# Optimization experiments

Measured on AMD Instinct MI355X. Metric: run time of the kernel, lower is better.

The kernel has to match this reference:

```python
import jax, jax.numpy as jnp
import numpy as np

B, L, D = 4, 2048, 64
N_HEAD = 4
LOCALITY = 0.2
PI = 3.141592653589793


def setup_inputs() -> dict:
    key = jax.random.key(0)
    k1, k2, k3 = jax.random.split(key, 3)
    mesh = jax.random.uniform(k1, (B, L, 2), dtype=jnp.float32)
    inputs = jax.random.normal(k2, (B, L, D), dtype=jnp.float32)
    lmda = jax.random.uniform(k3, (N_HEAD, 1, 1), dtype=jnp.float32)
    return {"mesh": mesh, "inputs": inputs, "lmda": lmda}


def reference(mesh, inputs, lmda):
    FMAX = jnp.finfo(jnp.float32).max
    # pairwise squared distances: (B, L, L)
    diff = mesh[:, :, None, :] - mesh[:, None, :, :]
    m_dist = jnp.sum(diff * diff, axis=-1)
    # per-head scale in (0, inf): tan(pi/4 * (1-eps) * (1 + sin(lmda)))
    scale = jnp.tan(0.25 * PI * (1.0 - 1e-07) * (1.0 + jnp.sin(lmda)))  # (H,1,1)
    scaled = m_dist[:, None, :, :] * scale  # (B, H, L, L)
    # row-wise quantile threshold (linear interpolation, matching torch.quantile)
    thresh = jnp.quantile(scaled, LOCALITY, axis=-1, keepdims=True)  # (B,H,L,1)
    masked = jnp.where(scaled <= thresh, scaled, FMAX)
    att = jax.nn.softmax(-masked, axis=-1)  # (B, H, L, L)
    # aggregate: (B,H,L,L) x (B,L,D) -> (B,L,H,D) -> (B,L,H*D)
    conv = jnp.einsum('bhnj,bjd->bnhd', att, inputs)
    conv = conv.reshape(inputs.shape[0], -1, N_HEAD * inputs.shape[-1])
    return jnp.concatenate([inputs, conv], axis=-1)
```

## Files before the change

### kernel.cpp

```cpp
#include <hip/hip_runtime.h>
#include <math.h>

#ifndef M_PI
#define M_PI 3.14159265358979323846
#endif

namespace {
constexpr int B_ = 4;
constexpr int L_ = 2048;
constexpr int D_ = 64;
constexpr int H_ = 4;
constexpr int RB = 16;
constexpr int KT = 64;
constexpr int NTILE = L_ / KT;
constexpr int CAPC = 256;
constexpr int OUTW = D_ + H_ * D_;
constexpr int APS = 2064;
}

typedef __attribute__((ext_vector_type(8))) short bf16x8;
typedef __attribute__((ext_vector_type(4))) float f32x4;

__device__ __forceinline__ unsigned bf16_rne(float x) {
    unsigned u = __float_as_uint(x);
    return (u + 0x7fffu + ((u >> 16) & 1u)) >> 16;
}

#define LDS_FENCE() __builtin_amdgcn_s_waitcnt(0xC07F)

__global__ __launch_bounds__(512, 8) void posatt_kernel(
    const float* __restrict__ mesh,
    const float* __restrict__ inputs,
    const float* __restrict__ lmda,
    float* __restrict__ out)
{
    __shared__ __align__(16) float2 s_mesh[L_];
    __shared__ __align__(16) char s_u1[16448];
    __shared__ float s_scale[H_];
    __shared__ float s_th[RB][H_];
    __shared__ float s_d409[RB], s_d410[RB];
    __shared__ float s_wsum[RB][H_];
    __shared__ unsigned s_ccw[8];

    const int t = threadIdx.x;
    const int l = t & 63;
    const int w = t >> 6;
    const int blk = blockIdx.x;
    const int b = blk >> 7;
    const int n0 = (blk & 127) * RB;

    if (t < H_) {
        const double lam = (double)lmda[t];
        const float C = (float)(0.25 * M_PI * (1.0 - 1e-07));
        const float s1 = (float)sin(lam);
        const float arg = __fmul_rn(C, __fadd_rn(1.0f, s1));
        s_scale[t] = (float)tan((double)arg);
    }
    {
        const float4* mg = reinterpret_cast<const float4*>(mesh + (size_t)b * L_ * 2);
        float4* msd = reinterpret_cast<float4*>(s_mesh);
        msd[t] = mg[t];
        msd[t + 512] = mg[t + 512];
    }
    __syncthreads();

    {
        unsigned* hw = reinterpret_cast<unsigned*>(s_u1) + w * 256;
        float* cw = reinterpret_cast<float*>(s_u1 + 8192) + w * CAPC;
        for (int rr = 0; rr < 2; ++rr) {
            const int rl = w * 2 + rr;
            const float2 me = s_mesh[n0 + rl];
            *reinterpret_cast<uint4*>(&hw[l * 4]) = make_uint4(0u, 0u, 0u, 0u);
            if (l == 0) s_ccw[w] = 0u;
            LDS_FENCE();
            #pragma unroll 1
            for (int it = 0; it < 32; ++it) {
                const int j = (it << 6) + l;
                const float2 mj = s_mesh[j];
                const float dx = __fsub_rn(me.x, mj.x);
                const float dy = __fsub_rn(me.y, mj.y);
                const float d = __fadd_rn(__fmul_rn(dx, dx), __fmul_rn(dy, dy));
                int bin = (int)(d * 128.0f); bin = bin < 255 ? bin : 255;
                atomicAdd(&hw[bin], 1u);
            }
            LDS_FENCE();
            const uint4 hv = *reinterpret_cast<const uint4*>(&hw[l * 4]);
            const unsigned p0 = hv.x, p1 = p0 + hv.y, p2 = p1 + hv.z, p3 = p2 + hv.w;
            unsigned sc = p3;
            #pragma unroll
            for (int off = 1; off < 64; off <<= 1) {
                const unsigned uu = __shfl_up(sc, off);
                if (l >= off) sc += uu;
            }
            const unsigned eb = sc - p3;
            const unsigned cum[4] = {eb + p0, eb + p1, eb + p2, eb + p3};
            int flo = -1, fhi = -1; unsigned fbase = 0u;
            #pragma unroll
            for (int e = 0; e < 4; ++e) {
                const unsigned prev = e ? cum[e - 1] : eb;
                if (cum[e] > 409u && prev <= 409u) { flo = l * 4 + e; fbase = prev; }
                if (cum[e] > 410u && prev <= 410u) { fhi = l * 4 + e; }
            }
            const unsigned long long bmlo = __ballot(flo >= 0);
            const int srclo = (int)__builtin_ctzll(bmlo);
            const int lo = __shfl(flo, srclo);
            const unsigned base = __shfl(fbase, srclo);
            const unsigned long long bmhi = __ballot(fhi >= 0);
            const int hi = __shfl(fhi, (int)__builtin_ctzll(bmhi));
            #pragma unroll 1
            for (int it = 0; it < 32; ++it) {
                const int j = (it << 6) + l;
                const float2 mj = s_mesh[j];
                const float dx = __fsub_rn(me.x, mj.x);
                const float dy = __fsub_rn(me.y, mj.y);
                const float d = __fadd_rn(__fmul_rn(dx, dx), __fmul_rn(dy, dy));
                int bin = (int)(d * 128.0f); bin = bin < 255 ? bin : 255;
                if (bin >= lo && bin <= hi) {
                    const unsigned p = atomicAdd(&s_ccw[w], 1u);
                    if (p < (unsigned)CAPC) cw[p] = d;
                }
            }
            LDS_FENCE();
            const int m = (int)min(s_ccw[w], (unsigned)CAPC);
            const int k409 = 409 - (int)base;
            const int k410 = 410 - (int)base;
            #pragma unroll 1
            for (int cc0 = 0; cc0 < m; cc0 += 64) {
                const int ci = cc0 + l;
                const float v = (ci < m) ? cw[ci] : 0.0f;
                int lt = 0, le = 0;
                #pragma unroll 1
                for (int i = 0; i < m; ++i) {
                    const float u = cw[i];
                    lt += (u < v) ? 1 : 0;
                    le += (u <= v) ? 1 : 0;
                }
                if (ci < m) {
                    if (lt <= k409 && k409 < le) s_d409[rl] = v;
                    if (lt <= k410 && k410 < le) s_d410[rl] = v;
                }
            }
            LDS_FENCE();
        }
    }
    __syncthreads();

    if (t < RB * H_) {
        const int r = t >> 2, h = t & 3;
        const float scl = s_scale[h];
        const float s409 = __fmul_rn(s_d409[r], scl);
        const float s410 = __fmul_rn(s_d410[r], scl);
        const float pos = 0.2f * 2047.0f;
        const float g = pos - 409.0f;
        const float lw = 1.0f - g;
        s_th[r][h] = __fadd_rn(__fmul_rn(s409, lw), __fmul_rn(s410, g));
    }
    __syncthreads();

    const int rl_b = t >> 5;
    const int h_b  = (t >> 3) & 3;
    const int jg   = t & 7;
    const float2 me_b = s_mesh[n0 + rl_b];
    const float sc_b = s_scale[h_b];
    const float th_b = s_th[rl_b][h_b];
    float wacc = 0.0f;

    const int hw_ = w >> 1;
    const int kq  = w & 1;
    f32x4 acc[4];
    #pragma unroll
    for (int nq = 0; nq < 4; ++nq) acc[nq] = (f32x4)0.0f;

    const float* inpb = inputs + (size_t)b * L_ * D_;
    char* Abase = s_u1;
    char* Bbase = s_u1 + 4 * APS;

    #pragma unroll 1
    for (int tile = 0; tile < NTILE; ++tile) {
        __syncthreads();
        unsigned pk0[4];
        {
            const int kb0 = tile * KT + ((t >> 6) << 3);
            const float* pb0 = inpb + (size_t)kb0 * D_ + (t & 63);
            #pragma unroll
            for (int e2 = 0; e2 < 4; ++e2) {
                const float xa = pb0[(2 * e2) * D_];
                const float xb = pb0[(2 * e2 + 1) * D_];
                pk0[e2] = bf16_rne(xa) | (bf16_rne(xb) << 16);
            }
        }
        const int k0 = tile * KT;
        #pragma unroll
        for (int m = 0; m < 4; ++m) {
            const int jl = (m << 4) + (jg << 1);
            const float4 mq = *reinterpret_cast<const float4*>(&s_mesh[k0 + jl]);
            const float dx0 = __fsub_rn(me_b.x, mq.x);
            const float dy0 = __fsub_rn(me_b.y, mq.y);
            const float d0 = __fadd_rn(__fmul_rn(dx0, dx0), __fmul_rn(dy0, dy0));
            const float dx1 = __fsub_rn(me_b.x, mq.z);
            const float dy1 = __fsub_rn(me_b.y, mq.w);
            const float d1 = __fadd_rn(__fmul_rn(dx1, dx1), __fmul_rn(dy1, dy1));
            const float x0 = __fmul_rn(d0, sc_b);
            const float x1 = __fmul_rn(d1, sc_b);
            const float e0 = __expf(-x0);
            const float e1 = __expf(-x1);
            const float w0 = (x0 <= th_b) ? e0 : 0.0f;
            const float w1 = (x1 <= th_b) ? e1 : 0.0f;
            wacc += w0 + w1;
            const unsigned u0 = bf16_rne(w0);
            const unsigned u1 = bf16_rne(w1);
            const int ktl = m >> 1;
            const int ql = ((m << 1) + (jg >> 2)) & 3;
            const int chunk = (ktl * 4 + ql) * 16 + rl_b;
            *reinterpret_cast<unsigned*>(Abase + h_b * APS + chunk * 16 + ((jg & 3) << 2)) = u0 | (u1 << 16);
        }
        *reinterpret_cast<uint4*>(Bbase + t * 16) = make_uint4(pk0[0], pk0[1], pk0[2], pk0[3]);
        __syncthreads();
        bf16x8 bfr[4];
        #pragma unroll
        for (int nq = 0; nq < 4; ++nq) {
            bfr[nq] = *reinterpret_cast<const bf16x8*>(
                Bbase + ((kq * 4 + (l >> 4)) * 64 + nq * 16 + (l & 15)) * 16);
        }
        const bf16x8 afr = *reinterpret_cast<const bf16x8*>(
            Abase + hw_ * APS + ((kq * 4 + (l >> 4)) * 16 + (l & 15)) * 16);
        #pragma unroll
        for (int nq = 0; nq < 4; ++nq) {
            acc[nq] = __builtin_amdgcn_mfma_f32_16x16x32_bf16(afr, bfr[nq], acc[nq], 0, 0, 0);
        }
    }
    __syncthreads();

    wacc += __shfl_xor(wacc, 1);
    wacc += __shfl_xor(wacc, 2);
    wacc += __shfl_xor(wacc, 4);
    if ((l & 7) == 0) s_wsum[rl_b][h_b] = wacc;
    {
        float4* Cz = reinterpret_cast<float4*>(s_u1);
        Cz[t] = make_float4(0.f, 0.f, 0.f, 0.f);
        Cz[t + 512] = make_float4(0.f, 0.f, 0.f, 0.f);
    }
    __syncthreads();
    {
        float* Cf = reinterpret_cast<float*>(s_u1);
        #pragma unroll
        for (int nq = 0; nq < 4; ++nq) {
            #pragma unroll
            for (int reg = 0; reg < 4; ++reg) {
                const int row = (l >> 4) * 4 + reg;
                const int col = l & 15;
                atomicAdd(&Cf[((hw_ * 4 + nq) * 16 + row) * 16 + col], acc[nq][reg]);
            }
        }
    }
    __syncthreads();
    {
        const float* Cf = reinterpret_cast<const float*>(s_u1);
        const int r = t >> 5;
        const int c0 = (t & 31) << 3;
        const int h = c0 >> 6;
        const int nq = (c0 >> 4) & 3;
        const int cl = c0 & 15;
        const float wsv = s_wsum[r][h];
        const float inv = (wsv != 0.0f) ? 1.0f / wsv : 0.0f;
        const float* src = &Cf[((h * 4 + nq) * 16 + r) * 16 + cl];
        float4 r0 = *reinterpret_cast<const float4*>(src);
        float4 r1 = *reinterpret_cast<const float4*>(src + 4);
        r0.x *= inv; r0.y *= inv; r0.z *= inv; r0.w *= inv;
        r1.x *= inv; r1.y *= inv; r1.z *= inv; r1.w *= inv;
        float* op = out + (size_t)(b * L_ + n0 + r) * OUTW + D_ + c0;
        *reinterpret_cast<float4*>(op) = r0;
        *reinterpret_cast<float4*>(op + 4) = r1;
    }
    {
        const int r = t >> 5;
        const int c0 = (t & 31) << 1;
        const float2 v = *reinterpret_cast<const float2*>(
            inputs + ((size_t)b * L_ + n0 + r) * D_ + c0);
        *reinterpret_cast<float2*>(out + (size_t)(b * L_ + n0 + r) * OUTW + c0) = v;
    }
}

extern "C" void kernel_launch(void* const* d_in, const int* in_sizes, int n_in,
                              void* d_out, int out_size, void* d_ws, size_t ws_size,
                              hipStream_t stream) {
    const float* mesh   = (const float*)d_in[0];
    const float* inputs = (const float*)d_in[1];
    const float* lmda   = (const float*)d_in[2];
    float* out = (float*)d_out;
    (void)in_sizes; (void)n_in; (void)out_size; (void)d_ws; (void)ws_size;
    hipLaunchKernelGGL(posatt_kernel, dim3(B_ * (L_ / RB)), dim3(512), 0, stream,
                       mesh, inputs, lmda, out);
}
```

Baseline: 145.1 us.

## Halve rows per block and pack two heads into each 16-row MFMA tile

Rows per block drop from 16 to 8, which doubles the grid to 1024 blocks. Each wave now computes the quantile threshold for a single row instead of two. The MFMA A operand is rebuilt so two heads' 8 rows fill one 16-row tile, and waves split along head-pair, K-half and N-half. The aim is to shorten each block's serial threshold phase and spread the work over more CUs, at the cost of reloading mesh and the input tiles twice as often across blocks.

```diff
diff --git a/kernel.cpp b/kernel.cpp
--- a/kernel.cpp
+++ b/kernel.cpp
@@ -10,7 +10,7 @@
 constexpr int L_ = 2048;
 constexpr int D_ = 64;
 constexpr int H_ = 4;
-constexpr int RB = 16;
+constexpr int RB = 8;
 constexpr int KT = 64;
 constexpr int NTILE = L_ / KT;
 constexpr int CAPC = 256;
@@ -46,8 +46,8 @@
     const int l = t & 63;
     const int w = t >> 6;
     const int blk = blockIdx.x;
-    const int b = blk >> 7;
-    const int n0 = (blk & 127) * RB;
+    const int b = blk >> 8;
+    const int n0 = (blk & 255) * RB;
 
     if (t < H_) {
         const double lam = (double)lmda[t];
@@ -67,80 +67,77 @@
     {
         unsigned* hw = reinterpret_cast<unsigned*>(s_u1) + w * 256;
         float* cw = reinterpret_cast<float*>(s_u1 + 8192) + w * CAPC;
-        for (int rr = 0; rr < 2; ++rr) {
-            const int rl = w * 2 + rr;
-            const float2 me = s_mesh[n0 + rl];
-            *reinterpret_cast<uint4*>(&hw[l * 4]) = make_uint4(0u, 0u, 0u, 0u);
-            if (l == 0) s_ccw[w] = 0u;
-            LDS_FENCE();
+        const int rl = w;
+        const float2 me = s_mesh[n0 + rl];
+        *reinterpret_cast<uint4*>(&hw[l * 4]) = make_uint4(0u, 0u, 0u, 0u);
+        if (l == 0) s_ccw[w] = 0u;
+        LDS_FENCE();
+        #pragma unroll 1
+        for (int it = 0; it < 32; ++it) {
+            const int j = (it << 6) + l;
+            const float2 mj = s_mesh[j];
+            const float dx = __fsub_rn(me.x, mj.x);
+            const float dy = __fsub_rn(me.y, mj.y);
+            const float d = __fadd_rn(__fmul_rn(dx, dx), __fmul_rn(dy, dy));
+            int bin = (int)(d * 128.0f); bin = bin < 255 ? bin : 255;
+            atomicAdd(&hw[bin], 1u);
+        }
+        LDS_FENCE();
+        const uint4 hv = *reinterpret_cast<const uint4*>(&hw[l * 4]);
+        const unsigned p0 = hv.x, p1 = p0 + hv.y, p2 = p1 + hv.z, p3 = p2 + hv.w;
+        unsigned sc = p3;
+        #pragma unroll
+        for (int off = 1; off < 64; off <<= 1) {
+            const unsigned uu = __shfl_up(sc, off);
+            if (l >= off) sc += uu;
+        }
+        const unsigned eb = sc - p3;
+        const unsigned cum[4] = {eb + p0, eb + p1, eb + p2, eb + p3};
+        int flo = -1, fhi = -1; unsigned fbase = 0u;
+        #pragma unroll
+        for (int e = 0; e < 4; ++e) {
+            const unsigned prev = e ? cum[e - 1] : eb;
+            if (cum[e] > 409u && prev <= 409u) { flo = l * 4 + e; fbase = prev; }
+            if (cum[e] > 410u && prev <= 410u) { fhi = l * 4 + e; }
+        }
+        const unsigned long long bmlo = __ballot(flo >= 0);
+        const int srclo = (int)__builtin_ctzll(bmlo);
+        const int lo = __shfl(flo, srclo);
+        const unsigned base = __shfl(fbase, srclo);
+        const unsigned long long bmhi = __ballot(fhi >= 0);
+        const int hi = __shfl(fhi, (int)__builtin_ctzll(bmhi));
+        #pragma unroll 1
+        for (int it = 0; it < 32; ++it) {
+            const int j = (it << 6) + l;
+            const float2 mj = s_mesh[j];
+            const float dx = __fsub_rn(me.x, mj.x);
+            const float dy = __fsub_rn(me.y, mj.y);
+            const float d = __fadd_rn(__fmul_rn(dx, dx), __fmul_rn(dy, dy));
+            int bin = (int)(d * 128.0f); bin = bin < 255 ? bin : 255;
+            if (bin >= lo && bin <= hi) {
+                const unsigned p = atomicAdd(&s_ccw[w], 1u);
+                if (p < (unsigned)CAPC) cw[p] = d;
+            }
+        }
+        LDS_FENCE();
+        const int m = (int)min(s_ccw[w], (unsigned)CAPC);
+        const int k409 = 409 - (int)base;
+        const int k410 = 410 - (int)base;
+        #pragma unroll 1
+        for (int cc0 = 0; cc0 < m; cc0 += 64) {
+            const int ci = cc0 + l;
+            const float v = (ci < m) ? cw[ci] : 0.0f;
+            int lt = 0, le = 0;
             #pragma unroll 1
-            for (int it = 0; it < 32; ++it) {
-                const int j = (it << 6) + l;
-                const float2 mj = s_mesh[j];
-                const float dx = __fsub_rn(me.x, mj.x);
-                const float dy = __fsub_rn(me.y, mj.y);
-                const float d = __fadd_rn(__fmul_rn(dx, dx), __fmul_rn(dy, dy));
-                int bin = (int)(d * 128.0f); bin = bin < 255 ? bin : 255;
-                atomicAdd(&hw[bin], 1u);
-            }
-            LDS_FENCE();
-            const uint4 hv = *reinterpret_cast<const uint4*>(&hw[l * 4]);
-            const unsigned p0 = hv.x, p1 = p0 + hv.y, p2 = p1 + hv.z, p3 = p2 + hv.w;
-            unsigned sc = p3;
-            #pragma unroll
-            for (int off = 1; off < 64; off <<= 1) {
-                const unsigned uu = __shfl_up(sc, off);
-                if (l >= off) sc += uu;
-            }
-            const unsigned eb = sc - p3;
-            const unsigned cum[4] = {eb + p0, eb + p1, eb + p2, eb + p3};
-            int flo = -1, fhi = -1; unsigned fbase = 0u;
-            #pragma unroll
-            for (int e = 0; e < 4; ++e) {
-                const unsigned prev = e ? cum[e - 1] : eb;
-                if (cum[e] > 409u && prev <= 409u) { flo = l * 4 + e; fbase = prev; }
-                if (cum[e] > 410u && prev <= 410u) { fhi = l * 4 + e; }
-            }
-            const unsigned long long bmlo = __ballot(flo >= 0);
-            const int srclo = (int)__builtin_ctzll(bmlo);
-            const int lo = __shfl(flo, srclo);
-            const unsigned base = __shfl(fbase, srclo);
-            const unsigned long long bmhi = __ballot(fhi >= 0);
-            const int hi = __shfl(fhi, (int)__builtin_ctzll(bmhi));
-            #pragma unroll 1
-            for (int it = 0; it < 32; ++it) {
-                const int j = (it << 6) + l;
-                const float2 mj = s_mesh[j];
-                const float dx = __fsub_rn(me.x, mj.x);
-                const float dy = __fsub_rn(me.y, mj.y);
-                const float d = __fadd_rn(__fmul_rn(dx, dx), __fmul_rn(dy, dy));
-                int bin = (int)(d * 128.0f); bin = bin < 255 ? bin : 255;
-                if (bin >= lo && bin <= hi) {
-                    const unsigned p = atomicAdd(&s_ccw[w], 1u);
-                    if (p < (unsigned)CAPC) cw[p] = d;
-                }
-            }
-            LDS_FENCE();
-            const int m = (int)min(s_ccw[w], (unsigned)CAPC);
-            const int k409 = 409 - (int)base;
-            const int k410 = 410 - (int)base;
-            #pragma unroll 1
-            for (int cc0 = 0; cc0 < m; cc0 += 64) {
-                const int ci = cc0 + l;
-                const float v = (ci < m) ? cw[ci] : 0.0f;
-                int lt = 0, le = 0;
-                #pragma unroll 1
-                for (int i = 0; i < m; ++i) {
-                    const float u = cw[i];
-                    lt += (u < v) ? 1 : 0;
-                    le += (u <= v) ? 1 : 0;
-                }
-                if (ci < m) {
-                    if (lt <= k409 && k409 < le) s_d409[rl] = v;
-                    if (lt <= k410 && k410 < le) s_d410[rl] = v;
-                }
-            }
-            LDS_FENCE();
+            for (int i = 0; i < m; ++i) {
+                const float u = cw[i];
+                lt += (u < v) ? 1 : 0;
+                le += (u <= v) ? 1 : 0;
+            }
+            if (ci < m) {
+                if (lt <= k409 && k409 < le) s_d409[rl] = v;
+                if (lt <= k410 && k410 < le) s_d410[rl] = v;
+            }
         }
     }
     __syncthreads();
@@ -157,23 +154,27 @@
     }
     __syncthreads();
 
-    const int rl_b = t >> 5;
-    const int h_b  = (t >> 3) & 3;
-    const int jg   = t & 7;
-    const float2 me_b = s_mesh[n0 + rl_b];
+    const int mr   = t >> 4;
+    const int h_b  = mr >> 3;
+    const int r_b  = mr & 7;
+    const int jg   = t & 15;
+    const int row16 = ((h_b & 1) << 3) + r_b;
+    const int pln   = h_b >> 1;
+    const float2 me_b = s_mesh[n0 + r_b];
     const float sc_b = s_scale[h_b];
-    const float th_b = s_th[rl_b][h_b];
+    const float th_b = s_th[r_b][h_b];
+    const int aoff = pln * APS + ((((jg >> 3) * 4 + ((jg >> 1) & 3)) * 16 + row16) << 4) + ((jg & 1) << 3);
     float wacc = 0.0f;
 
-    const int hw_ = w >> 1;
-    const int kq  = w & 1;
-    f32x4 acc[4];
-    #pragma unroll
-    for (int nq = 0; nq < 4; ++nq) acc[nq] = (f32x4)0.0f;
+    const int p_w  = w >> 2;
+    const int ks_w = (w >> 1) & 1;
+    const int nqh  = w & 1;
+    f32x4 acc[2];
+    acc[0] = (f32x4)0.0f; acc[1] = (f32x4)0.0f;
 
     const float* inpb = inputs + (size_t)b * L_ * D_;
     char* Abase = s_u1;
-    char* Bbase = s_u1 + 4 * APS;
+    char* Bbase = s_u1 + 2 * APS;
 
     #pragma unroll 1
     for (int tile = 0; tile < NTILE; ++tile) {
@@ -190,43 +191,44 @@
             }
         }
         const int k0 = tile * KT;
-        #pragma unroll
-        for (int m = 0; m < 4; ++m) {
-            const int jl = (m << 4) + (jg << 1);
-            const float4 mq = *reinterpret_cast<const float4*>(&s_mesh[k0 + jl]);
-            const float dx0 = __fsub_rn(me_b.x, mq.x);
-            const float dy0 = __fsub_rn(me_b.y, mq.y);
+        {
+            const float4 mq0 = *reinterpret_cast<const float4*>(&s_mesh[k0 + jg * 4]);
+            const float4 mq1 = *reinterpret_cast<const float4*>(&s_mesh[k0 + jg * 4 + 2]);
+            const float dx0 = __fsub_rn(me_b.x, mq0.x);
+            const float dy0 = __fsub_rn(me_b.y, mq0.y);
             const float d0 = __fadd_rn(__fmul_rn(dx0, dx0), __fmul_rn(dy0, dy0));
-            const float dx1 = __fsub_rn(me_b.x, mq.z);
-            const float dy1 = __fsub_rn(me_b.y, mq.w);
+            const float dx1 = __fsub_rn(me_b.x, mq0.z);
+            const float dy1 = __fsub_rn(me_b.y, mq0.w);
             const float d1 = __fadd_rn(__fmul_rn(dx1, dx1), __fmul_rn(dy1, dy1));
+            const float dx2 = __fsub_rn(me_b.x, mq1.x);
+            const float dy2 = __fsub_rn(me_b.y, mq1.y);
+            const float d2 = __fadd_rn(__fmul_rn(dx2, dx2), __fmul_rn(dy2, dy2));
+            const float dx3 = __fsub_rn(me_b.x, mq1.z);
+            const float dy3 = __fsub_rn(me_b.y, mq1.w);
+            const float d3 = __fadd_rn(__fmul_rn(dx3, dx3), __fmul_rn(dy3, dy3));
             const float x0 = __fmul_rn(d0, sc_b);
             const float x1 = __fmul_rn(d1, sc_b);
-            const float e0 = __expf(-x0);
-            const float e1 = __expf(-x1);
-            const float w0 = (x0 <= th_b) ? e0 : 0.0f;
-            const float w1 = (x1 <= th_b) ? e1 : 0.0f;
-            wacc += w0 + w1;
-            const unsigned u0 = bf16_rne(w0);
-            const unsigned u1 = bf16_rne(w1);
-            const int ktl = m >> 1;
-            const int ql = ((m << 1) + (jg >> 2)) & 3;
-            const int chunk = (ktl * 4 + ql) * 16 + rl_b;
-            *reinterpret_cast<unsigned*>(Abase + h_b * APS + chunk * 16 + ((jg & 3) << 2)) = u0 | (u1 << 16);
+            const float x2 = __fmul_rn(d2, sc_b);
+            const float x3 = __fmul_rn(d3, sc_b);
+            const float w0 = (x0 <= th_b) ? __expf(-x0) : 0.0f;
+            const float w1 = (x1 <= th_b) ? __expf(-x1) : 0.0f;
+            const float w2 = (x2 <= th_b) ? __expf(-x2) : 0.0f;
+            const float w3 = (x3 <= th_b) ? __expf(-x3) : 0.0f;
+            wacc += (w0 + w1) + (w2 + w3);
+            const unsigned u01 = bf16_rne(w0) | (bf16_rne(w1) << 16);
+            const unsigned u23 = bf16_rne(w2) | (bf16_rne(w3) << 16);
+            *reinterpret_cast<uint2*>(Abase + aoff) = make_uint2(u01, u23);
         }
         *reinterpret_cast<uint4*>(Bbase + t * 16) = make_uint4(pk0[0], pk0[1], pk0[2], pk0[3]);
         __syncthreads();
-        bf16x8 bfr[4];
-        #pragma unroll
-        for (int nq = 0; nq < 4; ++nq) {
-            bfr[nq] = *reinterpret_cast<const bf16x8*>(
-                Bbase + ((kq * 4 + (l >> 4)) * 64 + nq * 16 + (l & 15)) * 16);
-        }
         const bf16x8 afr = *reinterpret_cast<const bf16x8*>(
-            Abase + hw_ * APS + ((kq * 4 + (l >> 4)) * 16 + (l & 15)) * 16);
-        #pragma unroll
-        for (int nq = 0; nq < 4; ++nq) {
-            acc[nq] = __builtin_amdgcn_mfma_f32_16x16x32_bf16(afr, bfr[nq], acc[nq], 0, 0, 0);
+            Abase + p_w * APS + (((ks_w * 4 + (l >> 4)) * 16 + (l & 15)) << 4));
+        #pragma unroll
+        for (int i = 0; i < 2; ++i) {
+            const int nq = nqh * 2 + i;
+            const bf16x8 bfr = *reinterpret_cast<const bf16x8*>(
+                Bbase + (((ks_w * 4 + (l >> 4)) * 64 + nq * 16 + (l & 15)) << 4));
+            acc[i] = __builtin_amdgcn_mfma_f32_16x16x32_bf16(afr, bfr, acc[i], 0, 0, 0);
         }
     }
     __syncthreads();
@@ -234,50 +236,46 @@
     wacc += __shfl_xor(wacc, 1);
     wacc += __shfl_xor(wacc, 2);
     wacc += __shfl_xor(wacc, 4);
-    if ((l & 7) == 0) s_wsum[rl_b][h_b] = wacc;
+    wacc += __shfl_xor(wacc, 8);
+    if ((l & 15) == 0) s_wsum[r_b][h_b] = wacc;
     {
         float4* Cz = reinterpret_cast<float4*>(s_u1);
         Cz[t] = make_float4(0.f, 0.f, 0.f, 0.f);
-        Cz[t + 512] = make_float4(0.f, 0.f, 0.f, 0.f);
     }
     __syncthreads();
     {
         float* Cf = reinterpret_cast<float*>(s_u1);
         #pragma unroll
-        for (int nq = 0; nq < 4; ++nq) {
+        for (int i = 0; i < 2; ++i) {
+            const int nq = nqh * 2 + i;
             #pragma unroll
             for (int reg = 0; reg < 4; ++reg) {
                 const int row = (l >> 4) * 4 + reg;
-                const int col = l & 15;
-                atomicAdd(&Cf[((hw_ * 4 + nq) * 16 + row) * 16 + col], acc[nq][reg]);
+                const int col = nq * 16 + (l & 15);
+                atomicAdd(&Cf[(p_w * 16 + row) * 64 + col], acc[i][reg]);
             }
         }
     }
     __syncthreads();
     {
         const float* Cf = reinterpret_cast<const float*>(s_u1);
-        const int r = t >> 5;
-        const int c0 = (t & 31) << 3;
-        const int h = c0 >> 6;
-        const int nq = (c0 >> 4) & 3;
-        const int cl = c0 & 15;
+        const int pr = t >> 4;
+        const int p = pr >> 4;
+        const int row16o = pr & 15;
+        const int h = p * 2 + (row16o >> 3);
+        const int r = row16o & 7;
+        const int col = (t & 15) << 2;
         const float wsv = s_wsum[r][h];
         const float inv = (wsv != 0.0f) ? 1.0f / wsv : 0.0f;
-        const float* src = &Cf[((h * 4 + nq) * 16 + r) * 16 + cl];
-        float4 r0 = *reinterpret_cast<const float4*>(src);
-        float4 r1 = *reinterpret_cast<const float4*>(src + 4);
+        float4 r0 = *reinterpret_cast<const float4*>(&Cf[pr * 64 + col]);
         r0.x *= inv; r0.y *= inv; r0.z *= inv; r0.w *= inv;
-        r1.x *= inv; r1.y *= inv; r1.z *= inv; r1.w *= inv;
-        float* op = out + (size_t)(b * L_ + n0 + r) * OUTW + D_ + c0;
+        float* op = out + (size_t)(b * L_ + n0 + r) * OUTW + D_ + h * 64 + col;
         *reinterpret_cast<float4*>(op) = r0;
-        *reinterpret_cast<float4*>(op + 4) = r1;
-    }
-    {
-        const int r = t >> 5;
-        const int c0 = (t & 31) << 1;
-        const float2 v = *reinterpret_cast<const float2*>(
-            inputs + ((size_t)b * L_ + n0 + r) * D_ + c0);
-        *reinterpret_cast<float2*>(out + (size_t)(b * L_ + n0 + r) * OUTW + c0) = v;
+    }
+    {
+        const int r = t >> 6;
+        const int c = t & 63;
+        out[(size_t)(b * L_ + n0 + r) * OUTW + c] = inpb[(size_t)(n0 + r) * D_ + c];
     }
 }
 
```

Result: no change. 146.5 us (+1.0%).
